# Kernel tuning notes

Hardware: AMD Instinct MI355X
Metric: run time of the kernel (lower is better)

Reference implementation:

```python
import jax, jax.numpy as jnp
import numpy as np

START_TAG = 7
STOP_TAG = 8
NEG = -10000.0  # matches torch.full((1,K), -10000.) in the original


def setup_inputs() -> dict:
    key = jax.random.key(0)
    k1, k2, k3, k4 = jax.random.split(key, 4)
    B, T, K = 1024, 2048, 9  # K = output_dim + 2 (START/STOP hardcoded as 7/8)
    feats = jax.random.normal(k1, (B, T, K), dtype=jnp.float32)
    tags = jax.random.randint(k2, (B, T), 0, 7)            # valid labels 0..6
    lengths = jax.random.randint(k3, (B,), 1, T + 1)        # per-sentence lengths >= 1
    transitions = jax.random.normal(k4, (K, K), dtype=jnp.float32)
    transitions = transitions.at[START_TAG, :].set(NEG)     # never transition into START
    transitions = transitions.at[:, STOP_TAG].set(NEG)      # never transition out of STOP
    return {"feats": feats, "transitions": transitions, "tags": tags, "lengths": lengths}


def _crf_nll(feats, transitions, tags, lengths):
    # feats: [B,T,K] emissions, transitions[j,i] = score of i -> j
    B, T, K = feats.shape

    def fwd_one(feat, length):
        # CRF forward algorithm (log partition), vectorized over tags,
        # lax.scan over time; masked past `length` to emulate feats[:x_len].
        alpha0 = jnp.full((K,), NEG, feat.dtype).at[START_TAG].set(0.0)

        def step(alpha, inp):
            t, f = inp
            # alpha_new[j] = logsumexp_i(alpha[i] + transitions[j,i]) + feat[t,j]
            new = jax.nn.logsumexp(alpha[None, :] + transitions, axis=1) + f
            return jnp.where(t < length, new, alpha), None

        alpha, _ = jax.lax.scan(step, alpha0, (jnp.arange(T), feat))
        return jax.nn.logsumexp(alpha + transitions[STOP_TAG])

    fwd_scores = jax.vmap(fwd_one)(feats, lengths)  # [B]

    def gold_one(feat, tg, length):
        # _score_sentence: sum_t trans[tags[t], tags[t-1]] + feat[t, tags[t]]
        prev = jnp.concatenate([jnp.array([START_TAG], tg.dtype), tg[:-1]])
        step_scores = transitions[tg, prev] + jnp.take_along_axis(feat, tg[:, None], axis=1)[:, 0]
        mask = jnp.arange(tg.shape[0]) < length
        last = tg[length - 1]
        return jnp.sum(jnp.where(mask, step_scores, 0.0)) + transitions[STOP_TAG, last]

    gold_scores = jax.vmap(gold_one)(feats, tags, lengths)  # [B]

    # neg_log_likelihood accumulates (forward - gold) per sentence, then / n
    return jnp.mean(fwd_scores - gold_scores)


def reference(feats, transitions, tags, lengths):
    return _crf_nll(feats, transitions, tags, lengths)
```

## Files before the change

kernel.cpp:

```cpp
#include <hip/hip_runtime.h>


#define START_TAG 7
#define STOP_TAG  8
#define KDIM      9
#define NS        7
#define CHUNKS    32
#define NEGINF    (-1e30f)

__device__ __forceinline__ float rfl(float x) {
    return __int_as_float(__builtin_amdgcn_readfirstlane(__float_as_int(x)));
}

__global__ __launch_bounds__(256) void crf_fused_kernel(
    const float* __restrict__ feats,
    const float* __restrict__ trans,
    const int*   __restrict__ tags,
    const int*   __restrict__ lengths,
    float* __restrict__ out,
    int B, int T, int L)
{
    __shared__ float s_trans[81];
    __shared__ float s_E[49];
    __shared__ float s_M[CHUNKS * 64];
    __shared__ float s_gold[4];

    const int tid = threadIdx.x;
    const int b   = blockIdx.x;

    if (tid < 81) s_trans[tid] = trans[tid];
    if (tid >= 128 && tid < 128 + 49) {
        int k = tid - 128;
        s_E[k] = __expf(trans[(k / 7) * 9 + (k % 7)]);
    }
    __syncthreads();

    const int    len   = lengths[b];
    const int*   tg    = tags  + (size_t)b * T;
    const float* fbase = feats + (size_t)b * T * KDIM;

    {
        int per = T >> 8;
        int t0  = tid * per;
        float g = 0.f;
        if (t0 < len) {
            int te   = min(t0 + per, len);
            int prev = (t0 == 0) ? START_TAG : tg[t0 - 1];
            for (int t = t0; t < te; ++t) {
                int cur = tg[t];
                g += s_trans[cur * 9 + prev] + fbase[(size_t)t * KDIM + cur];
                prev = cur;
            }
            if (len - 1 < t0 + per) g += s_trans[STOP_TAG * 9 + tg[len - 1]];
        }
        #pragma unroll
        for (int off = 32; off > 0; off >>= 1) g += __shfl_xor(g, off, 64);
        if ((tid & 63) == 0) s_gold[tid >> 6] = g;
    }

    {
        const int lane8 = tid & 7;
        const int c     = tid >> 3;
        const int t0    = c * L;
        const int tstart = max(t0, 1);
        const int tend   = min(t0 + L, len);

        if (lane8 < NS) {
            const int col = lane8;
            float* Mw = s_M + c * 64;
            if (tstart < tend) {
                float E[49];
                #pragma unroll
                for (int k = 0; k < 49; ++k) E[k] = rfl(s_E[k]);

                float p[NS];
                #pragma unroll
                for (int j = 0; j < NS; ++j) p[j] = (j == col) ? 1.f : 0.f;
                float s = 0.f;

                const float* fp = fbase + (size_t)tstart * KDIM;
                int steps = tend - tstart;

                #define CRF_STEP() do {                                         \
                    float4 fA = *(const float4*)fp;                             \
                    float4 fB = *(const float4*)(fp + 4);                       \
                    fp += KDIM;                                                 \
                    float f[NS] = {fA.x, fA.y, fA.z, fA.w, fB.x, fB.y, fB.z};   \
                    float q[NS];                                                \
                    _Pragma("unroll")                                           \
                    for (int j = 0; j < NS; ++j) {                              \
                        float acc = E[j * 7] * p[0];                            \
                        _Pragma("unroll")                                       \
                        for (int i = 1; i < NS; ++i)                            \
                            acc = fmaf(E[j * 7 + i], p[i], acc);                \
                        q[j] = acc * __expf(f[j]);                              \
                    }                                                           \
                    _Pragma("unroll")                                           \
                    for (int j = 0; j < NS; ++j) p[j] = q[j];                   \
                } while (0)

                #define CRF_RENORM() do {                                       \
                    float m = p[0];                                             \
                    _Pragma("unroll")                                           \
                    for (int j = 1; j < NS; ++j) m = fmaxf(m, p[j]);            \
                    float rm = __builtin_amdgcn_rcpf(m);                        \
                    _Pragma("unroll")                                           \
                    for (int j = 0; j < NS; ++j) p[j] *= rm;                    \
                    s += __logf(m);                                             \
                } while (0)

                while (steps >= 4) {
                    CRF_STEP(); CRF_STEP(); CRF_STEP(); CRF_STEP();
                    CRF_RENORM();
                    steps -= 4;
                }
                if (steps > 0) {
                    while (steps-- > 0) { CRF_STEP(); }
                    CRF_RENORM();
                }

                #pragma unroll
                for (int j = 0; j < NS; ++j)
                    Mw[j * 8 + col] = __logf(p[j]) + s;
            } else {
                #pragma unroll
                for (int j = 0; j < NS; ++j)
                    Mw[j * 8 + col] = (j == col) ? 0.f : NEGINF;
            }
        }
    }
    __syncthreads();

    if (tid < 8) {
        const int lane = tid;
        const bool isrow = (lane < NS);
        const int row = isrow ? lane : 0;

        float a, S;
        {
            float a0 = isrow ? (s_trans[lane * 9 + START_TAG] + fbase[lane]) : NEGINF;
            float m = a0;
            #pragma unroll
            for (int off = 4; off > 0; off >>= 1) m = fmaxf(m, __shfl_xor(m, off, 8));
            a = a0 - m;
            S = m;
        }

        const int nc = (len + L - 1) / L;
        for (int c = 0; c < nc; ++c) {
            const float* Mr = s_M + c * 64 + row * 8;
            float tv[NS];
            float tm = NEGINF;
            #pragma unroll
            for (int i = 0; i < NS; ++i) {
                float ai = __shfl(a, i, 8);
                tv[i] = Mr[i] + ai;
                tm = fmaxf(tm, tv[i]);
            }
            float sum = 0.f;
            #pragma unroll
            for (int i = 0; i < NS; ++i) sum += __expf(tv[i] - tm);
            float na = tm + __logf(sum);
            float m2 = na;
            #pragma unroll
            for (int off = 4; off > 0; off >>= 1) m2 = fmaxf(m2, __shfl_xor(m2, off, 8));
            a = na - m2;
            S += m2;
        }

        float term = isrow ? (a + s_trans[STOP_TAG * 9 + lane]) : NEGINF;
        float tm2 = term;
        #pragma unroll
        for (int off = 4; off > 0; off >>= 1) tm2 = fmaxf(tm2, __shfl_xor(tm2, off, 8));
        float e = isrow ? __expf(term - tm2) : 0.f;
        #pragma unroll
        for (int off = 4; off > 0; off >>= 1) e += __shfl_xor(e, off, 8);

        if (lane == 0) {
            float fwd = S + tm2 + __logf(e);
            float g = s_gold[0] + s_gold[1] + s_gold[2] + s_gold[3];
            atomicAdd(out, (fwd - g) * (1.0f / (float)B));
        }
    }
}

__global__ void init_out_kernel(float* out) {
    if (threadIdx.x == 0) out[0] = 0.f;
}

extern "C" void kernel_launch(void* const* d_in, const int* in_sizes, int n_in,
                              void* d_out, int out_size, void* d_ws, size_t ws_size,
                              hipStream_t stream) {
    const float* feats   = (const float*)d_in[0];
    const float* trans   = (const float*)d_in[1];
    const int*   tags    = (const int*)d_in[2];
    const int*   lengths = (const int*)d_in[3];

    int B = in_sizes[3];
    int T = in_sizes[2] / B;
    int L = (T + CHUNKS - 1) / CHUNKS;

    init_out_kernel<<<1, 64, 0, stream>>>((float*)d_out);
    crf_fused_kernel<<<B, 256, 0, stream>>>(
        feats, trans, tags, lengths, (float*)d_out, B, T, L);
}
```

Before: 167.6 us.

## Split CRF into chunk-scan, tree-combine, and reduce kernels with prefetched feats

Moves the per-chunk transfer-matrix scan into its own 64-thread kernel with small blocks, launch bounds for occupancy, and a three-deep register prefetch of emission rows. Chunk log-matrices now go through a global workspace. A second kernel combines them with a parallel log-semiring tree product instead of a serial 8-lane loop, and a third kernel replaces the atomic accumulation with a deterministic reduction. This adds a global write and re-read of the chunk matrices, two extra launches and higher register pressure in exchange for more parallelism and latency hiding.

```diff
diff --git a/kernel.cpp b/kernel.cpp
--- a/kernel.cpp
+++ b/kernel.cpp
@@ -3,189 +3,256 @@
 
 #define START_TAG 7
 #define STOP_TAG  8
-#define KDIM      9
-#define NS        7
-#define CHUNKS    32
-#define NEGINF    (-1e30f)
+#define KD     9
+#define NS     7
+#define CHUNKS 32
+#define SLOT   56
+#define NEG1   (-1e30f)
 
 __device__ __forceinline__ float rfl(float x) {
     return __int_as_float(__builtin_amdgcn_readfirstlane(__float_as_int(x)));
 }
 
-__global__ __launch_bounds__(256) void crf_fused_kernel(
+__global__ __launch_bounds__(64, 3) void crf_chunkA(
+    const float* __restrict__ feats,
+    const float* __restrict__ trans,
+    const int*   __restrict__ lengths,
+    float* __restrict__ logM,
+    int T, int L)
+{
+    float E[49];
+    #pragma unroll
+    for (int k = 0; k < 49; ++k)
+        E[k] = rfl(__expf(trans[(k / 7) * KD + (k % 7)]));
+
+    const int gtid  = blockIdx.x * 64 + threadIdx.x;
+    const int lane8 = gtid & 7;
+    const int grp   = gtid >> 3;
+    const int c     = grp & (CHUNKS - 1);
+    const int b     = grp >> 5;
+
+    const int len    = lengths[b];
+    const int t0     = c * L;
+    const int tstart = (t0 > 1) ? t0 : 1;
+    const int tend   = min(t0 + L, len);
+    const int n      = tend - tstart;
+    if (lane8 >= NS || n <= 0) return;
+
+    const float* fp = feats + ((size_t)b * T + tstart) * KD;
+
+    float p[NS];
+    #pragma unroll
+    for (int j = 0; j < NS; ++j) p[j] = (j == lane8) ? 1.f : 0.f;
+    float s = 0.f;
+
+    const int mb   = n >> 2;
+    const int tail = n & 3;
+    const int nm1  = n - 1;
+
+    float4 B0[8], B1[8], B2[8];
+
+    #define LOADB(DST, M) do {                                                  \
+        int r0_ = min(4*(M)+0, nm1), r1_ = min(4*(M)+1, nm1);                   \
+        int r2_ = min(4*(M)+2, nm1), r3_ = min(4*(M)+3, nm1);                   \
+        DST[0] = *(const float4*)(fp + r0_*KD); DST[1] = *(const float4*)(fp + r0_*KD + 4); \
+        DST[2] = *(const float4*)(fp + r1_*KD); DST[3] = *(const float4*)(fp + r1_*KD + 4); \
+        DST[4] = *(const float4*)(fp + r2_*KD); DST[5] = *(const float4*)(fp + r2_*KD + 4); \
+        DST[6] = *(const float4*)(fp + r3_*KD); DST[7] = *(const float4*)(fp + r3_*KD + 4); \
+    } while (0)
+
+    #define STEP(FA, FB) do {                                                   \
+        float ef[NS] = { __expf((FA).x), __expf((FA).y), __expf((FA).z),        \
+                         __expf((FA).w), __expf((FB).x), __expf((FB).y),        \
+                         __expf((FB).z) };                                      \
+        float q[NS];                                                            \
+        _Pragma("unroll")                                                       \
+        for (int j = 0; j < NS; ++j) {                                          \
+            float acc = E[j*7] * p[0];                                          \
+            _Pragma("unroll")                                                   \
+            for (int i = 1; i < NS; ++i) acc = fmaf(E[j*7+i], p[i], acc);       \
+            q[j] = acc;                                                         \
+        }                                                                       \
+        _Pragma("unroll")                                                       \
+        for (int j = 0; j < NS; ++j) p[j] = q[j] * ef[j];                       \
+    } while (0)
+
+    #define RENORM() do {                                                       \
+        float m = p[0];                                                         \
+        _Pragma("unroll")                                                       \
+        for (int j = 1; j < NS; ++j) m = fmaxf(m, p[j]);                        \
+        float rm = __builtin_amdgcn_rcpf(m);                                    \
+        _Pragma("unroll")                                                       \
+        for (int j = 0; j < NS; ++j) p[j] *= rm;                                \
+        s += __logf(m);                                                         \
+    } while (0)
+
+    LOADB(B0, 0);
+    LOADB(B1, 1);
+
+    for (int m = 0; m < mb; ++m) {
+        LOADB(B2, m + 2);
+        STEP(B0[0], B0[1]); STEP(B0[2], B0[3]);
+        STEP(B0[4], B0[5]); STEP(B0[6], B0[7]);
+        RENORM();
+        #pragma unroll
+        for (int k = 0; k < 8; ++k) { B0[k] = B1[k]; B1[k] = B2[k]; }
+    }
+    if (tail > 0) {
+        STEP(B0[0], B0[1]);
+        if (tail > 1) STEP(B0[2], B0[3]);
+        if (tail > 2) STEP(B0[4], B0[5]);
+        RENORM();
+    }
+
+    float* outp = logM + (size_t)grp * SLOT + lane8 * 8;
+    #pragma unroll
+    for (int j = 0; j < NS; ++j)
+        outp[j] = fmaxf(__logf(p[j]), NEG1) + s;
+
+    #undef LOADB
+    #undef STEP
+    #undef RENORM
+}
+
+__global__ __launch_bounds__(256) void crf_combineB(
     const float* __restrict__ feats,
     const float* __restrict__ trans,
     const int*   __restrict__ tags,
     const int*   __restrict__ lengths,
-    float* __restrict__ out,
-    int B, int T, int L)
+    const float* __restrict__ logM,
+    float* __restrict__ perb,
+    int T, int L)
 {
     __shared__ float s_trans[81];
-    __shared__ float s_E[49];
-    __shared__ float s_M[CHUNKS * 64];
+    __shared__ float s_mat[CHUNKS * 64];
+    __shared__ float s_buf[(CHUNKS / 2) * 64];
     __shared__ float s_gold[4];
+    __shared__ float s_alpha0[8];
 
     const int tid = threadIdx.x;
     const int b   = blockIdx.x;
+    const int len = lengths[b];
+    const float* fbase = feats + (size_t)b * T * KD;
+    const int*   tg    = tags  + (size_t)b * T;
 
     if (tid < 81) s_trans[tid] = trans[tid];
-    if (tid >= 128 && tid < 128 + 49) {
-        int k = tid - 128;
-        s_E[k] = __expf(trans[(k / 7) * 9 + (k % 7)]);
-    }
     __syncthreads();
 
-    const int    len   = lengths[b];
-    const int*   tg    = tags  + (size_t)b * T;
-    const float* fbase = feats + (size_t)b * T * KDIM;
-
     {
-        int per = T >> 8;
+        int per = (T >> 8) > 0 ? (T >> 8) : 1;
         int t0  = tid * per;
         float g = 0.f;
         if (t0 < len) {
             int te   = min(t0 + per, len);
             int prev = (t0 == 0) ? START_TAG : tg[t0 - 1];
-            for (int t = t0; t < te; ++t) {
-                int cur = tg[t];
-                g += s_trans[cur * 9 + prev] + fbase[(size_t)t * KDIM + cur];
+            for (int k = 0; k < per; ++k) {
+                int t   = t0 + k;
+                int tc  = min(t, te - 1);
+                int cur = tg[tc];
+                float v = s_trans[cur * KD + prev] + fbase[(size_t)tc * KD + cur];
+                g += (t < te) ? v : 0.f;
                 prev = cur;
             }
-            if (len - 1 < t0 + per) g += s_trans[STOP_TAG * 9 + tg[len - 1]];
+            if (len - 1 >= t0 && len - 1 < t0 + per)
+                g += s_trans[STOP_TAG * KD + tg[len - 1]];
         }
         #pragma unroll
         for (int off = 32; off > 0; off >>= 1) g += __shfl_xor(g, off, 64);
         if ((tid & 63) == 0) s_gold[tid >> 6] = g;
     }
 
-    {
-        const int lane8 = tid & 7;
-        const int c     = tid >> 3;
-        const int t0    = c * L;
-        const int tstart = max(t0, 1);
-        const int tend   = min(t0 + L, len);
-
-        if (lane8 < NS) {
-            const int col = lane8;
-            float* Mw = s_M + c * 64;
-            if (tstart < tend) {
-                float E[49];
-                #pragma unroll
-                for (int k = 0; k < 49; ++k) E[k] = rfl(s_E[k]);
-
-                float p[NS];
-                #pragma unroll
-                for (int j = 0; j < NS; ++j) p[j] = (j == col) ? 1.f : 0.f;
-                float s = 0.f;
-
-                const float* fp = fbase + (size_t)tstart * KDIM;
-                int steps = tend - tstart;
-
-                #define CRF_STEP() do {                                         \
-                    float4 fA = *(const float4*)fp;                             \
-                    float4 fB = *(const float4*)(fp + 4);                       \
-                    fp += KDIM;                                                 \
-                    float f[NS] = {fA.x, fA.y, fA.z, fA.w, fB.x, fB.y, fB.z};   \
-                    float q[NS];                                                \
-                    _Pragma("unroll")                                           \
-                    for (int j = 0; j < NS; ++j) {                              \
-                        float acc = E[j * 7] * p[0];                            \
-                        _Pragma("unroll")                                       \
-                        for (int i = 1; i < NS; ++i)                            \
-                            acc = fmaf(E[j * 7 + i], p[i], acc);                \
-                        q[j] = acc * __expf(f[j]);                              \
-                    }                                                           \
-                    _Pragma("unroll")                                           \
-                    for (int j = 0; j < NS; ++j) p[j] = q[j];                   \
-                } while (0)
-
-                #define CRF_RENORM() do {                                       \
-                    float m = p[0];                                             \
-                    _Pragma("unroll")                                           \
-                    for (int j = 1; j < NS; ++j) m = fmaxf(m, p[j]);            \
-                    float rm = __builtin_amdgcn_rcpf(m);                        \
-                    _Pragma("unroll")                                           \
-                    for (int j = 0; j < NS; ++j) p[j] *= rm;                    \
-                    s += __logf(m);                                             \
-                } while (0)
-
-                while (steps >= 4) {
-                    CRF_STEP(); CRF_STEP(); CRF_STEP(); CRF_STEP();
-                    CRF_RENORM();
-                    steps -= 4;
-                }
-                if (steps > 0) {
-                    while (steps-- > 0) { CRF_STEP(); }
-                    CRF_RENORM();
-                }
-
-                #pragma unroll
-                for (int j = 0; j < NS; ++j)
-                    Mw[j * 8 + col] = __logf(p[j]) + s;
-            } else {
-                #pragma unroll
-                for (int j = 0; j < NS; ++j)
-                    Mw[j * 8 + col] = (j == col) ? 0.f : NEGINF;
-            }
+    if (tid < 8)
+        s_alpha0[tid] = (tid < NS) ? (s_trans[tid * KD + START_TAG] + fbase[tid]) : NEG1;
+
+    for (int idx = tid; idx < CHUNKS * SLOT; idx += 256) {
+        int c = idx / SLOT, k = idx - c * SLOT;
+        bool act = (c == 0) ? (len > 1) : (c * L < len);
+        float v;
+        if (act) v = logM[(size_t)(b * CHUNKS + c) * SLOT + k];
+        else     v = ((k >> 3) == (k & 7)) ? 0.f : NEG1;
+        s_mat[c * 64 + k] = v;
+    }
+    __syncthreads();
+
+    const int  e    = tid >> 6;
+    const int  lane = tid & 63;
+    const int  j    = lane % 7;
+    const int  i    = lane / 7;
+    const bool actl = lane < 49;
+
+    #define PRODROUND(SRC, DST, P) do {                                         \
+        for (int p_ = e; p_ < (P); p_ += 4) {                                   \
+            const float* Lb = (SRC) + (2 * p_ + 1) * 64;                        \
+            const float* Rb = (SRC) + (2 * p_) * 64;                            \
+            if (actl) {                                                         \
+                float tv[NS];                                                   \
+                tv[0] = Lb[j] + Rb[i * 8];                                      \
+                float tm = tv[0];                                               \
+                _Pragma("unroll")                                               \
+                for (int k = 1; k < NS; ++k) {                                  \
+                    tv[k] = Lb[k * 8 + j] + Rb[i * 8 + k];                      \
+                    tm = fmaxf(tm, tv[k]);                                      \
+                }                                                               \
+                float sum = 0.f;                                                \
+                _Pragma("unroll")                                               \
+                for (int k = 0; k < NS; ++k) sum += __expf(tv[k] - tm);         \
+                (DST)[p_ * 64 + i * 8 + j] = tm + __logf(sum);                  \
+            }                                                                   \
+        }                                                                       \
+        __syncthreads();                                                        \
+    } while (0)
+
+    PRODROUND(s_mat, s_buf, 16);
+    PRODROUND(s_buf, s_mat, 8);
+    PRODROUND(s_mat, s_buf, 4);
+    PRODROUND(s_buf, s_mat, 2);
+    PRODROUND(s_mat, s_buf, 1);
+    #undef PRODROUND
+
+    if (tid < 8) {
+        const bool isrow = (tid < NS);
+        const int  jj    = isrow ? tid : 0;
+        float tv[NS];
+        tv[0] = s_buf[jj] + s_alpha0[0];
+        float tm = tv[0];
+        #pragma unroll
+        for (int i2 = 1; i2 < NS; ++i2) {
+            tv[i2] = s_buf[i2 * 8 + jj] + s_alpha0[i2];
+            tm = fmaxf(tm, tv[i2]);
         }
-    }
+        float sum = 0.f;
+        #pragma unroll
+        for (int i2 = 0; i2 < NS; ++i2) sum += __expf(tv[i2] - tm);
+        float af = tm + __logf(sum);
+
+        float term = isrow ? (af + s_trans[STOP_TAG * KD + tid]) : NEG1;
+        float tm2 = term;
+        #pragma unroll
+        for (int off = 4; off > 0; off >>= 1) tm2 = fmaxf(tm2, __shfl_xor(tm2, off, 8));
+        float ee = isrow ? __expf(term - tm2) : 0.f;
+        #pragma unroll
+        for (int off = 4; off > 0; off >>= 1) ee += __shfl_xor(ee, off, 8);
+
+        if (tid == 0) {
+            float fwd = tm2 + __logf(ee);
+            perb[b] = fwd - (s_gold[0] + s_gold[1] + s_gold[2] + s_gold[3]);
+        }
+    }
+}
+
+__global__ __launch_bounds__(256) void crf_reduceC(
+    const float* __restrict__ perb, float* __restrict__ out, int B)
+{
+    __shared__ float sd[256];
+    float s = 0.f;
+    for (int i = threadIdx.x; i < B; i += 256) s += perb[i];
+    sd[threadIdx.x] = s;
     __syncthreads();
-
-    if (tid < 8) {
-        const int lane = tid;
-        const bool isrow = (lane < NS);
-        const int row = isrow ? lane : 0;
-
-        float a, S;
-        {
-            float a0 = isrow ? (s_trans[lane * 9 + START_TAG] + fbase[lane]) : NEGINF;
-            float m = a0;
-            #pragma unroll
-            for (int off = 4; off > 0; off >>= 1) m = fmaxf(m, __shfl_xor(m, off, 8));
-            a = a0 - m;
-            S = m;
-        }
-
-        const int nc = (len + L - 1) / L;
-        for (int c = 0; c < nc; ++c) {
-            const float* Mr = s_M + c * 64 + row * 8;
-            float tv[NS];
-            float tm = NEGINF;
-            #pragma unroll
-            for (int i = 0; i < NS; ++i) {
-                float ai = __shfl(a, i, 8);
-                tv[i] = Mr[i] + ai;
-                tm = fmaxf(tm, tv[i]);
-            }
-            float sum = 0.f;
-            #pragma unroll
-            for (int i = 0; i < NS; ++i) sum += __expf(tv[i] - tm);
-            float na = tm + __logf(sum);
-            float m2 = na;
-            #pragma unroll
-            for (int off = 4; off > 0; off >>= 1) m2 = fmaxf(m2, __shfl_xor(m2, off, 8));
-            a = na - m2;
-            S += m2;
-        }
-
-        float term = isrow ? (a + s_trans[STOP_TAG * 9 + lane]) : NEGINF;
-        float tm2 = term;
-        #pragma unroll
-        for (int off = 4; off > 0; off >>= 1) tm2 = fmaxf(tm2, __shfl_xor(tm2, off, 8));
-        float e = isrow ? __expf(term - tm2) : 0.f;
-        #pragma unroll
-        for (int off = 4; off > 0; off >>= 1) e += __shfl_xor(e, off, 8);
-
-        if (lane == 0) {
-            float fwd = S + tm2 + __logf(e);
-            float g = s_gold[0] + s_gold[1] + s_gold[2] + s_gold[3];
-            atomicAdd(out, (fwd - g) * (1.0f / (float)B));
-        }
-    }
-}
-
-__global__ void init_out_kernel(float* out) {
-    if (threadIdx.x == 0) out[0] = 0.f;
+    for (int st = 128; st > 0; st >>= 1) {
+        if (threadIdx.x < st) sd[threadIdx.x] += sd[threadIdx.x + st];
+        __syncthreads();
+    }
+    if (threadIdx.x == 0) out[0] = sd[0] / (float)B;
 }
 
 extern "C" void kernel_launch(void* const* d_in, const int* in_sizes, int n_in,
@@ -200,7 +267,12 @@
     int T = in_sizes[2] / B;
     int L = (T + CHUNKS - 1) / CHUNKS;
 
-    init_out_kernel<<<1, 64, 0, stream>>>((float*)d_out);
-    crf_fused_kernel<<<B, 256, 0, stream>>>(
-        feats, trans, tags, lengths, (float*)d_out, B, T, L);
-}
+    float* logM = (float*)d_ws;
+    float* perb = logM + (size_t)B * CHUNKS * SLOT;
+
+    crf_chunkA<<<(B * CHUNKS * 8) / 64, 64, 0, stream>>>(
+        feats, trans, lengths, logM, T, L);
+    crf_combineB<<<B, 256, 0, stream>>>(
+        feats, trans, tags, lengths, logM, perb, T, L);
+    crf_reduceC<<<1, 256, 0, stream>>>(perb, (float*)d_out, B);
+}
```

Measured after the change: 164.6 us. About the same (-1.8%).
